# Kernel tuning notes

Measured on AMD Instinct MI355X. Metric: run time of the kernel, lower is better.

## Reference

```python
import jax, jax.numpy as jnp
import numpy as np

F_DIM = 128        # feature_dim
LATENT = 256       # latent_dim
HEADS = 4          # n_head
N_GRAPHS = 256
NODES_PER = 100    # < 180 (pos table size)
N = N_GRAPHS * NODES_PER
DEG = 8
E = N * DEG
MAX_POS = 180
NEG_SLOPE = 0.2


def sinusoid_table(n_node, d):
    pos = np.arange(n_node, dtype=np.float64)[:, None]
    j = np.arange(d, dtype=np.float64)[None, :]
    ang = pos / np.power(10000.0, 2.0 * (np.floor(j / 2.0)) / d)
    ang[:, 0::2] = np.sin(ang[:, 0::2])
    ang[:, 1::2] = np.cos(ang[:, 1::2])
    return jnp.asarray(ang, dtype=jnp.float32)  # [n_node, d]


def gat_layer(x, src, dst, W, a_src, a_dst, bias):
    # x: [N, in], W: [in, H*C], a_src/a_dst: [H, C], bias: [H*C]
    H, C = a_src.shape
    xl = (x @ W).reshape(N, H, C)                      # [N,H,C]
    s = jnp.einsum('nhc,hc->nh', xl, a_src)            # [N,H]
    d = jnp.einsum('nhc,hc->nh', xl, a_dst)            # [N,H]
    e = jax.nn.leaky_relu(s[src] + d[dst], NEG_SLOPE)  # [E,H]
    emax = jax.ops.segment_max(e, dst, num_segments=N)
    ex = jnp.exp(e - emax[dst])
    den = jax.ops.segment_sum(ex, dst, num_segments=N)
    alpha = ex / (den[dst] + 1e-16)                    # [E,H]
    out = jax.ops.segment_sum(alpha[:, :, None] * xl[src], dst, num_segments=N)
    return out.reshape(N, H * C) + bias


def setup_inputs() -> dict:
    key = jax.random.key(0)
    ks = jax.random.split(key, 20)
    sc = 0.05
    z = jax.random.normal(ks[0], (N_GRAPHS, LATENT), dtype=jnp.float32)
    batch = jnp.repeat(jnp.arange(N_GRAPHS, dtype=jnp.int64), NODES_PER)
    base = (jnp.arange(N, dtype=jnp.int64) // NODES_PER) * NODES_PER
    nbr = jax.random.randint(ks[1], (N, DEG), 0, NODES_PER, dtype=jnp.int64)
    src = (base[:, None] + nbr).reshape(-1)
    dst = jnp.repeat(jnp.arange(N, dtype=jnp.int64), DEG)
    edge_index = jnp.stack([src, dst], 0)
    HF = HEADS * F_DIM
    p = {
        'W0': jax.random.normal(ks[2], (LATENT, F_DIM)) * sc,
        'b0': jnp.zeros((F_DIM,), jnp.float32),
        'W1': jax.random.normal(ks[3], (2 * F_DIM, HF)) * sc,
        'as1': jax.random.normal(ks[4], (HEADS, F_DIM)) * sc,
        'ad1': jax.random.normal(ks[5], (HEADS, F_DIM)) * sc,
        'b1': jnp.zeros((HF,), jnp.float32),
        'W2': jax.random.normal(ks[6], (HF, HF)) * sc,
        'as2': jax.random.normal(ks[7], (HEADS, F_DIM)) * sc,
        'ad2': jax.random.normal(ks[8], (HEADS, F_DIM)) * sc,
        'b2': jnp.zeros((HF,), jnp.float32),
        'W3': jax.random.normal(ks[9], (HF, HF)) * sc,
        'as3': jax.random.normal(ks[10], (HEADS, F_DIM)) * sc,
        'ad3': jax.random.normal(ks[11], (HEADS, F_DIM)) * sc,
        'b3': jnp.zeros((HF,), jnp.float32),
        'Wg': jax.random.normal(ks[12], (HF, F_DIM)) * sc,
        'bg': jnp.zeros((F_DIM,), jnp.float32),
        'Wf': jax.random.normal(ks[13], (F_DIM, 5)) * sc,
        'bf': jnp.zeros((5,), jnp.float32),
    }
    return {'z': z, 'edge_index': edge_index, 'batch': batch, **p}


def reference(z, edge_index, batch, W0, b0, W1, as1, ad1, b1,
              W2, as2, ad2, b2, W3, as3, ad3, b3, Wg, bg, Wf, bf):
    # node order within each graph (intended semantics of node_order_within_batch)
    counts = jax.ops.segment_sum(jnp.ones((N,), jnp.int32), batch, num_segments=N_GRAPHS)
    cum = jnp.concatenate([jnp.zeros((1,), jnp.int32), jnp.cumsum(counts)[:-1]])
    order = jnp.arange(N, dtype=jnp.int32) - cum[batch]
    pos = sinusoid_table(MAX_POS, F_DIM)[order]        # [N, F]  (detached buffer)

    h = (z @ W0 + b0)[batch]                           # [N, F]
    h = jax.nn.relu(jnp.concatenate([h, pos], axis=1)) # [N, 2F]

    # PyG GATConv default add_self_loops=True
    loop = jnp.arange(N, dtype=edge_index.dtype)
    src = jnp.concatenate([edge_index[0], loop])
    dst = jnp.concatenate([edge_index[1], loop])

    h = jax.nn.relu(gat_layer(h, src, dst, W1, as1, ad1, b1))
    h = jax.nn.relu(gat_layer(h, src, dst, W2, as2, ad2, b2))
    h = jax.nn.relu(gat_layer(h, src, dst, W3, as3, ad3, b3))
    h = jax.nn.relu(h @ Wg + bg)
    return h @ Wf + bf                                 # [N, 5]
```

## Files before the change

### kernel.cpp

```cpp
#include <hip/hip_runtime.h>
#include <hip/hip_bf16.h>
#include <math.h>

#define N_GRAPHS 256
#define NODES_PER 100
#define NN (N_GRAPHS * NODES_PER)
#define DEG 8
#define FD 128
#define LAT 256
#define HFD 512
#define NEG_SLOPE 0.2f

typedef _Float16 half8 __attribute__((ext_vector_type(8)));
typedef float float4v __attribute__((ext_vector_type(4)));

__device__ __forceinline__ int xcd_swz(int bid, int total) {
    int q = total >> 3;
    return (bid & 7) * q + (bid >> 3);
}

__device__ __forceinline__ void gload_lds16(const _Float16* g, _Float16* l) {
    __builtin_amdgcn_global_load_lds(
        (const __attribute__((address_space(1))) unsigned int*)g,
        (__attribute__((address_space(3))) unsigned int*)l, 16, 0, 0);
}

__global__ void g0_kernel(const float* __restrict__ z, const float* __restrict__ W0,
                          const float* __restrict__ b0, float* __restrict__ g0) {
    __shared__ float s_z[LAT];
    int g = blockIdx.x;
    int j = threadIdx.x;
    s_z[j]       = z[g * LAT + j];
    s_z[j + 128] = z[g * LAT + 128 + j];
    __syncthreads();
    float acc = 0.f;
    #pragma unroll 8
    for (int k = 0; k < LAT; ++k)
        acc += s_z[k] * W0[k * FD + j];
    g0[g * FD + j] = acc + b0[j];
}

__global__ void build_x1_kernel(const float* __restrict__ g0,
                                const int* __restrict__ batch, _Float16* __restrict__ x1) {
    __shared__ int s_b, s_ord;
    int i = blockIdx.x;
    int t = threadIdx.x;
    if (t == 0) {
        int b = batch[i];
        int lo = 0, hi = i;
        while (lo < hi) { int mid = (lo + hi) >> 1; if (batch[mid] < b) lo = mid + 1; else hi = mid; }
        s_b = b;
        s_ord = i - lo;
    }
    __syncthreads();
    float v;
    if (t < 128) {
        v = g0[s_b * FD + t];
    } else {
        int j = t - 128;
        int j2 = j >> 1;
        float freq = expf(-(float)j2 * 0.1439115683f);
        float ang = (float)s_ord * freq;
        v = (j & 1) ? cosf(ang) : sinf(ang);
    }
    x1[(size_t)i * 256 + t] = (_Float16)fmaxf(v, 0.f);
}

__global__ void wconv_all_kernel(const float* __restrict__ W1, const float* __restrict__ W2,
                                 const float* __restrict__ W3, const float* __restrict__ Wg,
                                 _Float16* __restrict__ W1t, _Float16* __restrict__ W2t,
                                 _Float16* __restrict__ W3t, _Float16* __restrict__ Wgt) {
    __shared__ float tile[32][33];
    int b = blockIdx.x;
    const float* in; _Float16* out; int K, Nw, tid2;
    if (b < 128)      { in = W1; out = W1t; K = 256; Nw = 512; tid2 = b; }
    else if (b < 384) { in = W2; out = W2t; K = 512; Nw = 512; tid2 = b - 128; }
    else if (b < 640) { in = W3; out = W3t; K = 512; Nw = 512; tid2 = b - 384; }
    else              { in = Wg; out = Wgt; K = 512; Nw = 128; tid2 = b - 640; }
    int nxt = Nw / 32;
    int nb = (tid2 % nxt) * 32, kb = (tid2 / nxt) * 32;
    int tx = threadIdx.x & 31, ty = threadIdx.x >> 5;
    #pragma unroll
    for (int r = 0; r < 4; ++r)
        tile[ty + 8 * r][tx] = in[(size_t)(kb + ty + 8 * r) * Nw + nb + tx];
    __syncthreads();
    #pragma unroll
    for (int r = 0; r < 4; ++r)
        out[(size_t)(nb + ty + 8 * r) * K + kb + tx] = (_Float16)tile[tx][ty + 8 * r];
}

template <int K>
__global__ __launch_bounds__(512, 2) void gat_fused_kernel(
    const _Float16* __restrict__ X,
    const _Float16* __restrict__ Wt,
    const float* __restrict__ a_src,
    const float* __restrict__ a_dst,
    const int* __restrict__ esrc,
    const float* __restrict__ bias,
    _Float16* __restrict__ Xout) {
    __shared__ __align__(16) _Float16 As[128 * 32];
    __shared__ __align__(16) _Float16 Ylds[100 * 512];
    __shared__ float sdpart[112][8][2];
    __shared__ float s_lds[112][4];
    __shared__ float d_lds[112][4];

    const int g    = blockIdx.x;
    const int tid  = threadIdx.x;
    const int lane = tid & 63;
    const int wc   = tid >> 6;
    const int kq   = lane >> 4;
    const int l15  = lane & 15;
    const int rowbase = g * NODES_PER;

    const int srow = tid >> 2;
    const int sq   = (tid & 3) ^ ((tid >> 3) & 3);
    const _Float16* gA = X + (size_t)(rowbase + srow) * K + sq * 8;
    _Float16* ldsA = &As[wc * 512];

    const _Float16* gW[4];
    #pragma unroll
    for (int ni = 0; ni < 4; ++ni) {
        int c = wc * 64 + ni * 16 + l15;
        gW[ni] = Wt + (size_t)c * K + kq * 8;
    }

    float4v acc[7][4];
    #pragma unroll
    for (int mi = 0; mi < 7; ++mi)
        #pragma unroll
        for (int ni = 0; ni < 4; ++ni)
            acc[mi][ni] = (float4v){0.f, 0.f, 0.f, 0.f};

    const int nk = K >> 5;
    for (int ks = 0; ks < nk; ++ks) {
        gload_lds16(gA + ks * 32, ldsA);
        half8 bfr[4];
        #pragma unroll
        for (int ni = 0; ni < 4; ++ni)
            bfr[ni] = *(const half8*)(gW[ni] + ks * 32);
        __syncthreads();
        half8 af[7];
        #pragma unroll
        for (int mi = 0; mi < 7; ++mi) {
            int r = mi * 16 + l15;
            af[mi] = *(const half8*)&As[r * 32 + ((kq ^ ((r >> 1) & 3)) * 8)];
        }
        #pragma unroll
        for (int mi = 0; mi < 7; ++mi)
            #pragma unroll
            for (int ni = 0; ni < 4; ++ni)
                acc[mi][ni] = __builtin_amdgcn_mfma_f32_16x16x32_f16(af[mi], bfr[ni], acc[mi][ni], 0, 0, 0);
        __syncthreads();
    }

    float asv[4], adv[4];
    #pragma unroll
    for (int ni = 0; ni < 4; ++ni) {
        int c = wc * 64 + ni * 16 + l15;
        asv[ni] = a_src[c];
        adv[ni] = a_dst[c];
    }
    const int hi4 = lane >> 4;
    #pragma unroll
    for (int mi = 0; mi < 7; ++mi) {
        #pragma unroll
        for (int j = 0; j < 4; ++j) {
            int r = mi * 16 + hi4 * 4 + j;
            float ps = 0.f, pd = 0.f;
            #pragma unroll
            for (int ni = 0; ni < 4; ++ni) {
                float v = acc[mi][ni][j];
                ps += v * asv[ni];
                pd += v * adv[ni];
                if (r < NODES_PER) {
                    int c = wc * 64 + ni * 16 + l15;
                    Ylds[r * 512 + (((c >> 3) ^ (r & 7)) * 8) + (c & 7)] = (_Float16)v;
                }
            }
            #pragma unroll
            for (int m = 8; m >= 1; m >>= 1) {
                ps += __shfl_xor(ps, m);
                pd += __shfl_xor(pd, m);
            }
            if (l15 == 0) {
                sdpart[r][wc][0] = ps;
                sdpart[r][wc][1] = pd;
            }
        }
    }
    __syncthreads();
    if (tid < 448) {
        int r = tid >> 2, h = tid & 3;
        s_lds[r][h] = sdpart[r][2 * h][0] + sdpart[r][2 * h + 1][0];
        d_lds[r][h] = sdpart[r][2 * h][1] + sdpart[r][2 * h + 1][1];
    }
    __syncthreads();

    const int hd = lane >> 4;
    const int c0 = lane * 8;
    float4v b0 = *(const float4v*)&bias[c0];
    float4v b1 = *(const float4v*)&bias[c0 + 4];
    for (int i = wc; i < NODES_PER; i += 8) {
        int sg = (lane < 8) ? (esrc[(size_t)(rowbase + i) * DEG + lane] - rowbase) : i;
        int sl[9];
        #pragma unroll
        for (int k = 0; k < 9; ++k) sl[k] = __shfl(sg, k);
        float dh = d_lds[i][hd];
        float e[9];
        float mx = -1e30f;
        #pragma unroll
        for (int k = 0; k < 9; ++k) {
            float v = s_lds[sl[k]][hd] + dh;
            v = (v >= 0.f) ? v : NEG_SLOPE * v;
            e[k] = v;
            mx = fmaxf(mx, v);
        }
        float den = 0.f;
        #pragma unroll
        for (int k = 0; k < 9; ++k) { e[k] = __expf(e[k] - mx); den += e[k]; }
        float inv = 1.f / (den + 1e-16f);
        float a8[8] = {};
        #pragma unroll
        for (int k = 0; k < 9; ++k) {
            half8 y = *(const half8*)&Ylds[sl[k] * 512 + ((lane ^ (sl[k] & 7)) * 8)];
            float a = e[k] * inv;
            #pragma unroll
            for (int j = 0; j < 8; ++j) a8[j] += a * (float)y[j];
        }
        half8 o;
        #pragma unroll
        for (int j = 0; j < 4; ++j) {
            o[j]     = (_Float16)fmaxf(a8[j] + b0[j], 0.f);
            o[j + 4] = (_Float16)fmaxf(a8[j + 4] + b1[j], 0.f);
        }
        *(half8*)&Xout[(size_t)(rowbase + i) * HFD + c0] = o;
    }
}

__global__ __launch_bounds__(256) void head_kernel(
    const _Float16* __restrict__ X,
    const _Float16* __restrict__ Wt,
    const float* __restrict__ bias,
    const float* __restrict__ Wf,
    const float* __restrict__ bfv,
    float* __restrict__ out) {
    __shared__ __align__(16) _Float16 As[128 * 32];
    __shared__ __align__(16) _Float16 Bs[128 * 32];
    __shared__ float red[5][128][2];
    const int lin = xcd_swz(blockIdx.x, gridDim.x);
    const int row0 = lin * 128;
    const int tid  = threadIdx.x;
    const int lane = tid & 63;
    const int wave = tid >> 6;
    const int wm = wave >> 1;
    const int wn = wave & 1;
    const int K = 512;

    const int srow = tid >> 2;
    const int sq   = (tid & 3) ^ ((tid >> 3) & 3);
    const _Float16* gA0 = X  + (size_t)(row0 + srow) * K + sq * 8;
    const _Float16* gB0 = Wt + (size_t)srow * K + sq * 8;
    const _Float16* gA1 = gA0 + (size_t)64 * K;
    const _Float16* gB1 = gB0 + (size_t)64 * K;
    _Float16* ldsA0 = &As[wave * 512];
    _Float16* ldsA1 = &As[2048 + wave * 512];
    _Float16* ldsB0 = &Bs[wave * 512];
    _Float16* ldsB1 = &Bs[2048 + wave * 512];

    const int kq  = lane >> 4;
    const int l15 = lane & 15;

    float4v acc[4][4];
    #pragma unroll
    for (int i = 0; i < 4; ++i)
        #pragma unroll
        for (int j = 0; j < 4; ++j)
            acc[i][j] = (float4v){0.f, 0.f, 0.f, 0.f};

    for (int ks = 0; ks < 16; ++ks) {
        gload_lds16(gA0 + ks * 32, ldsA0);
        gload_lds16(gA1 + ks * 32, ldsA1);
        gload_lds16(gB0 + ks * 32, ldsB0);
        gload_lds16(gB1 + ks * 32, ldsB1);
        __syncthreads();
        half8 af[4], bfr[4];
        #pragma unroll
        for (int mi = 0; mi < 4; ++mi) {
            int r = wm * 64 + mi * 16 + l15;
            af[mi] = *(const half8*)&As[r * 32 + ((kq ^ ((r >> 1) & 3)) * 8)];
        }
        #pragma unroll
        for (int ni = 0; ni < 4; ++ni) {
            int c = wn * 64 + ni * 16 + l15;
            bfr[ni] = *(const half8*)&Bs[c * 32 + ((kq ^ ((c >> 1) & 3)) * 8)];
        }
        #pragma unroll
        for (int mi = 0; mi < 4; ++mi)
            #pragma unroll
            for (int ni = 0; ni < 4; ++ni)
                acc[mi][ni] = __builtin_amdgcn_mfma_f32_16x16x32_f16(af[mi], bfr[ni], acc[mi][ni], 0, 0, 0);
        __syncthreads();
    }

    float bgv[4], wf[4][5];
    #pragma unroll
    for (int ni = 0; ni < 4; ++ni) {
        int c = wn * 64 + ni * 16 + l15;
        bgv[ni] = bias[c];
        #pragma unroll
        for (int q = 0; q < 5; ++q) wf[ni][q] = Wf[c * 5 + q];
    }
    #pragma unroll
    for (int mi = 0; mi < 4; ++mi) {
        #pragma unroll
        for (int j = 0; j < 4; ++j) {
            float vr[4];
            #pragma unroll
            for (int ni = 0; ni < 4; ++ni)
                vr[ni] = fmaxf(acc[mi][ni][j] + bgv[ni], 0.f);
            #pragma unroll
            for (int q = 0; q < 5; ++q) {
                float p = vr[0] * wf[0][q] + vr[1] * wf[1][q] + vr[2] * wf[2][q] + vr[3] * wf[3][q];
                #pragma unroll
                for (int m = 8; m >= 1; m >>= 1) p += __shfl_xor(p, m);
                if (l15 == 0) {
                    int rloc = wm * 64 + mi * 16 + ((lane >> 4) << 2) + j;
                    red[q][rloc][wn] = p;
                }
            }
        }
    }
    __syncthreads();
    if (tid < 128) {
        #pragma unroll
        for (int q = 0; q < 5; ++q)
            out[(size_t)(row0 + tid) * 5 + q] = red[q][tid][0] + red[q][tid][1] + bfv[q];
    }
}

extern "C" void kernel_launch(void* const* d_in, const int* in_sizes, int n_in,
                              void* d_out, int out_size, void* d_ws, size_t ws_size,
                              hipStream_t stream) {
    const float* z    = (const float*)d_in[0];
    const int*  eidx  = (const int*)d_in[1];
    const int*  batch = (const int*)d_in[2];
    const float* W0  = (const float*)d_in[3];
    const float* b0  = (const float*)d_in[4];
    const float* W1  = (const float*)d_in[5];
    const float* as1 = (const float*)d_in[6];
    const float* ad1 = (const float*)d_in[7];
    const float* b1  = (const float*)d_in[8];
    const float* W2  = (const float*)d_in[9];
    const float* as2 = (const float*)d_in[10];
    const float* ad2 = (const float*)d_in[11];
    const float* b2  = (const float*)d_in[12];
    const float* W3  = (const float*)d_in[13];
    const float* as3 = (const float*)d_in[14];
    const float* ad3 = (const float*)d_in[15];
    const float* b3  = (const float*)d_in[16];
    const float* Wg  = (const float*)d_in[17];
    const float* bg  = (const float*)d_in[18];
    const float* Wf  = (const float*)d_in[19];
    const float* bfv = (const float*)d_in[20];
    float* out = (float*)d_out;

    float* ws   = (float*)d_ws;
    float* g0   = ws;
    _Float16* Xh1 = (_Float16*)(g0 + 32768);
    _Float16* Xa  = Xh1 + (size_t)NN * 256;
    _Float16* Xb  = Xa + (size_t)NN * 512;
    _Float16* W1t = Xb + (size_t)NN * 512;
    _Float16* W2t = W1t + 512 * 256;
    _Float16* W3t = W2t + 512 * 512;
    _Float16* Wgt = W3t + 512 * 512;

    g0_kernel<<<N_GRAPHS, FD, 0, stream>>>(z, W0, b0, g0);
    build_x1_kernel<<<NN, 256, 0, stream>>>(g0, batch, Xh1);
    wconv_all_kernel<<<704, 256, 0, stream>>>(W1, W2, W3, Wg, W1t, W2t, W3t, Wgt);

    gat_fused_kernel<256><<<N_GRAPHS, 512, 0, stream>>>(Xh1, W1t, as1, ad1, eidx, b1, Xa);
    gat_fused_kernel<512><<<N_GRAPHS, 512, 0, stream>>>(Xa,  W2t, as2, ad2, eidx, b2, Xb);
    gat_fused_kernel<512><<<N_GRAPHS, 512, 0, stream>>>(Xb,  W3t, as3, ad3, eidx, b3, Xa);

    head_kernel<<<NN / 128, 256, 0, stream>>>(Xa, Wgt, bg, Wf, bfv, out);
}
```

Before: 318.4 us.

## Split fused GAT kernel per graph into per-head blocks for more parallelism

Each fused GAT layer block now handles one (graph, head) pair instead of a whole graph. That gives 1024 blocks of 256 threads with a 128-column GEMM slice and a 100x128 LDS tile. The aim is more, smaller blocks with lower LDS use, so occupancy and load balance across CUs improve over 256 large blocks. In exchange, each head block reloads the graph's full input rows, and the block index is remapped so heads of the same graph land on the same XCD. Workspace buffers are padded because the GEMM reads rows past the graph end.

```diff
diff --git a/kernel.cpp b/kernel.cpp
--- a/kernel.cpp
+++ b/kernel.cpp
@@ -90,7 +90,7 @@
 }
 
 template <int K>
-__global__ __launch_bounds__(512, 2) void gat_fused_kernel(
+__global__ __launch_bounds__(256, 4) void gat2_kernel(
     const _Float16* __restrict__ X,
     const _Float16* __restrict__ Wt,
     const float* __restrict__ a_src,
@@ -99,45 +99,43 @@
     const float* __restrict__ bias,
     _Float16* __restrict__ Xout) {
     __shared__ __align__(16) _Float16 As[128 * 32];
-    __shared__ __align__(16) _Float16 Ylds[100 * 512];
-    __shared__ float sdpart[112][8][2];
-    __shared__ float s_lds[112][4];
-    __shared__ float d_lds[112][4];
-
-    const int g    = blockIdx.x;
+    __shared__ __align__(16) _Float16 Ylds[100 * 128];
+    __shared__ float sdp[112][4][2];
+    __shared__ float s_lds[112], d_lds[112];
+
+    const int b    = blockIdx.x;
+    const int g    = (b & 7) * 32 + ((b >> 3) >> 2);
+    const int h    = (b >> 3) & 3;
+    const int rowbase = g * NODES_PER;
     const int tid  = threadIdx.x;
     const int lane = tid & 63;
     const int wc   = tid >> 6;
     const int kq   = lane >> 4;
     const int l15  = lane & 15;
-    const int rowbase = g * NODES_PER;
 
     const int srow = tid >> 2;
     const int sq   = (tid & 3) ^ ((tid >> 3) & 3);
-    const _Float16* gA = X + (size_t)(rowbase + srow) * K + sq * 8;
-    _Float16* ldsA = &As[wc * 512];
-
-    const _Float16* gW[4];
-    #pragma unroll
-    for (int ni = 0; ni < 4; ++ni) {
-        int c = wc * 64 + ni * 16 + l15;
-        gW[ni] = Wt + (size_t)c * K + kq * 8;
-    }
-
-    float4v acc[7][4];
-    #pragma unroll
-    for (int mi = 0; mi < 7; ++mi)
-        #pragma unroll
-        for (int ni = 0; ni < 4; ++ni)
-            acc[mi][ni] = (float4v){0.f, 0.f, 0.f, 0.f};
+    const _Float16* gA0 = X + (size_t)(rowbase + srow) * K + sq * 8;
+    const _Float16* gA1 = gA0 + (size_t)64 * K;
+    _Float16* ldsA0 = &As[wc * 512];
+    _Float16* ldsA1 = &As[2048 + wc * 512];
+
+    const _Float16* gW0 = Wt + (size_t)(h * 128 + wc * 32 + l15) * K + kq * 8;
+    const _Float16* gW1 = gW0 + (size_t)16 * K;
+
+    float4v acc[7][2];
+    #pragma unroll
+    for (int mi = 0; mi < 7; ++mi) {
+        acc[mi][0] = (float4v){0.f, 0.f, 0.f, 0.f};
+        acc[mi][1] = (float4v){0.f, 0.f, 0.f, 0.f};
+    }
 
     const int nk = K >> 5;
     for (int ks = 0; ks < nk; ++ks) {
-        gload_lds16(gA + ks * 32, ldsA);
-        half8 bfr[4];
-        #pragma unroll
-        for (int ni = 0; ni < 4; ++ni)
-            bfr[ni] = *(const half8*)(gW[ni] + ks * 32);
+        gload_lds16(gA0 + ks * 32, ldsA0);
+        gload_lds16(gA1 + ks * 32, ldsA1);
+        half8 bf0 = *(const half8*)(gW0 + ks * 32);
+        half8 bf1 = *(const half8*)(gW1 + ks * 32);
         __syncthreads();
         half8 af[7];
         #pragma unroll
@@ -146,17 +144,17 @@
             af[mi] = *(const half8*)&As[r * 32 + ((kq ^ ((r >> 1) & 3)) * 8)];
         }
         #pragma unroll
-        for (int mi = 0; mi < 7; ++mi)
-            #pragma unroll
-            for (int ni = 0; ni < 4; ++ni)
-                acc[mi][ni] = __builtin_amdgcn_mfma_f32_16x16x32_f16(af[mi], bfr[ni], acc[mi][ni], 0, 0, 0);
+        for (int mi = 0; mi < 7; ++mi) {
+            acc[mi][0] = __builtin_amdgcn_mfma_f32_16x16x32_f16(af[mi], bf0, acc[mi][0], 0, 0, 0);
+            acc[mi][1] = __builtin_amdgcn_mfma_f32_16x16x32_f16(af[mi], bf1, acc[mi][1], 0, 0, 0);
+        }
         __syncthreads();
     }
 
-    float asv[4], adv[4];
-    #pragma unroll
-    for (int ni = 0; ni < 4; ++ni) {
-        int c = wc * 64 + ni * 16 + l15;
+    float asv[2], adv[2];
+    #pragma unroll
+    for (int ni = 0; ni < 2; ++ni) {
+        int c = h * 128 + wc * 32 + ni * 16 + l15;
         asv[ni] = a_src[c];
         adv[ni] = a_dst[c];
     }
@@ -166,15 +164,13 @@
         #pragma unroll
         for (int j = 0; j < 4; ++j) {
             int r = mi * 16 + hi4 * 4 + j;
-            float ps = 0.f, pd = 0.f;
-            #pragma unroll
-            for (int ni = 0; ni < 4; ++ni) {
-                float v = acc[mi][ni][j];
-                ps += v * asv[ni];
-                pd += v * adv[ni];
-                if (r < NODES_PER) {
-                    int c = wc * 64 + ni * 16 + l15;
-                    Ylds[r * 512 + (((c >> 3) ^ (r & 7)) * 8) + (c & 7)] = (_Float16)v;
+            float ps = acc[mi][0][j] * asv[0] + acc[mi][1][j] * asv[1];
+            float pd = acc[mi][0][j] * adv[0] + acc[mi][1][j] * adv[1];
+            if (r < NODES_PER) {
+                #pragma unroll
+                for (int ni = 0; ni < 2; ++ni) {
+                    int cl = wc * 32 + ni * 16 + l15;
+                    Ylds[r * 128 + (((cl >> 3) ^ (r & 15)) * 8) + (cl & 7)] = (_Float16)acc[mi][ni][j];
                 }
             }
             #pragma unroll
@@ -183,34 +179,38 @@
                 pd += __shfl_xor(pd, m);
             }
             if (l15 == 0) {
-                sdpart[r][wc][0] = ps;
-                sdpart[r][wc][1] = pd;
-            }
-        }
-    }
-    __syncthreads();
-    if (tid < 448) {
-        int r = tid >> 2, h = tid & 3;
-        s_lds[r][h] = sdpart[r][2 * h][0] + sdpart[r][2 * h + 1][0];
-        d_lds[r][h] = sdpart[r][2 * h][1] + sdpart[r][2 * h + 1][1];
-    }
-    __syncthreads();
-
-    const int hd = lane >> 4;
-    const int c0 = lane * 8;
-    float4v b0 = *(const float4v*)&bias[c0];
-    float4v b1 = *(const float4v*)&bias[c0 + 4];
-    for (int i = wc; i < NODES_PER; i += 8) {
-        int sg = (lane < 8) ? (esrc[(size_t)(rowbase + i) * DEG + lane] - rowbase) : i;
+                sdp[r][wc][0] = ps;
+                sdp[r][wc][1] = pd;
+            }
+        }
+    }
+    __syncthreads();
+    if (tid < 112) {
+        s_lds[tid] = sdp[tid][0][0] + sdp[tid][1][0] + sdp[tid][2][0] + sdp[tid][3][0];
+        d_lds[tid] = sdp[tid][0][1] + sdp[tid][1][1] + sdp[tid][2][1] + sdp[tid][3][1];
+    }
+    __syncthreads();
+
+    const int gl   = lane >> 4;
+    const int lsub = lane & 15;
+    const int shfb = lane & 48;
+    float4v bb0 = *(const float4v*)&bias[h * 128 + lsub * 8];
+    float4v bb1 = *(const float4v*)&bias[h * 128 + lsub * 8 + 4];
+    #pragma unroll
+    for (int it = 0; it < 7; ++it) {
+        int i = it * 16 + wc * 4 + gl;
+        bool act = (i < NODES_PER);
+        int ii = act ? i : (NODES_PER - 1);
+        int sg = (lsub < 8) ? (esrc[(size_t)(rowbase + ii) * DEG + lsub] - rowbase) : ii;
         int sl[9];
         #pragma unroll
-        for (int k = 0; k < 9; ++k) sl[k] = __shfl(sg, k);
-        float dh = d_lds[i][hd];
+        for (int k = 0; k < 9; ++k) sl[k] = __shfl(sg, shfb + k);
+        float dh = d_lds[ii];
         float e[9];
         float mx = -1e30f;
         #pragma unroll
         for (int k = 0; k < 9; ++k) {
-            float v = s_lds[sl[k]][hd] + dh;
+            float v = s_lds[sl[k]] + dh;
             v = (v >= 0.f) ? v : NEG_SLOPE * v;
             e[k] = v;
             mx = fmaxf(mx, v);
@@ -222,18 +222,20 @@
         float a8[8] = {};
         #pragma unroll
         for (int k = 0; k < 9; ++k) {
-            half8 y = *(const half8*)&Ylds[sl[k] * 512 + ((lane ^ (sl[k] & 7)) * 8)];
+            half8 y = *(const half8*)&Ylds[sl[k] * 128 + ((lsub ^ (sl[k] & 15)) * 8)];
             float a = e[k] * inv;
             #pragma unroll
             for (int j = 0; j < 8; ++j) a8[j] += a * (float)y[j];
         }
-        half8 o;
-        #pragma unroll
-        for (int j = 0; j < 4; ++j) {
-            o[j]     = (_Float16)fmaxf(a8[j] + b0[j], 0.f);
-            o[j + 4] = (_Float16)fmaxf(a8[j + 4] + b1[j], 0.f);
-        }
-        *(half8*)&Xout[(size_t)(rowbase + i) * HFD + c0] = o;
+        if (act) {
+            half8 o;
+            #pragma unroll
+            for (int j = 0; j < 4; ++j) {
+                o[j]     = (_Float16)fmaxf(a8[j] + bb0[j], 0.f);
+                o[j + 4] = (_Float16)fmaxf(a8[j + 4] + bb1[j], 0.f);
+            }
+            *(half8*)&Xout[(size_t)(rowbase + i) * HFD + h * 128 + lsub * 8] = o;
+        }
     }
 }
 
@@ -367,9 +369,9 @@
     float* ws   = (float*)d_ws;
     float* g0   = ws;
     _Float16* Xh1 = (_Float16*)(g0 + 32768);
-    _Float16* Xa  = Xh1 + (size_t)NN * 256;
-    _Float16* Xb  = Xa + (size_t)NN * 512;
-    _Float16* W1t = Xb + (size_t)NN * 512;
+    _Float16* Xa  = Xh1 + (size_t)(NN + 128) * 256;
+    _Float16* Xb  = Xa + (size_t)(NN + 128) * 512;
+    _Float16* W1t = Xb + (size_t)(NN + 128) * 512;
     _Float16* W2t = W1t + 512 * 256;
     _Float16* W3t = W2t + 512 * 512;
     _Float16* Wgt = W3t + 512 * 512;
@@ -378,9 +380,9 @@
     build_x1_kernel<<<NN, 256, 0, stream>>>(g0, batch, Xh1);
     wconv_all_kernel<<<704, 256, 0, stream>>>(W1, W2, W3, Wg, W1t, W2t, W3t, Wgt);
 
-    gat_fused_kernel<256><<<N_GRAPHS, 512, 0, stream>>>(Xh1, W1t, as1, ad1, eidx, b1, Xa);
-    gat_fused_kernel<512><<<N_GRAPHS, 512, 0, stream>>>(Xa,  W2t, as2, ad2, eidx, b2, Xb);
-    gat_fused_kernel<512><<<N_GRAPHS, 512, 0, stream>>>(Xb,  W3t, as3, ad3, eidx, b3, Xa);
+    gat2_kernel<256><<<N_GRAPHS * 4, 256, 0, stream>>>(Xh1, W1t, as1, ad1, eidx, b1, Xa);
+    gat2_kernel<512><<<N_GRAPHS * 4, 256, 0, stream>>>(Xa,  W2t, as2, ad2, eidx, b2, Xb);
+    gat2_kernel<512><<<N_GRAPHS * 4, 256, 0, stream>>>(Xb,  W3t, as3, ad3, eidx, b3, Xa);
 
     head_kernel<<<NN / 128, 256, 0, stream>>>(Xa, Wgt, bg, Wf, bfv, out);
 }
```

Measured after the change: 314.3 us. Within noise of the previous version (-1.3%).
